# Kernel optimization log

Hardware: AMD Instinct MI355X
Metric: run time of the kernel (lower is better)

The kernel has to match this reference:

```python
import jax, jax.numpy as jnp
from jax import lax
import numpy as np

B, N, H, T, NPB = 1024, 50, 128, 50, 3
C_TANH, NEG = 10.0, 1e9


def _lstm(x, h, c, Wi, Wh, b):
    gates = x @ Wi + h @ Wh + b
    i, f, g, o = jnp.split(gates, 4, axis=-1)
    c2 = jax.nn.sigmoid(f) * c + jax.nn.sigmoid(i) * jnp.tanh(g)
    return jax.nn.sigmoid(o) * jnp.tanh(c2), c2


def setup_inputs() -> dict:
    key = jax.random.key(0)
    ks = jax.random.split(key, 20)
    rn = lambda k, shape, fan: (jax.random.normal(k, shape, jnp.float32) / np.float32(np.sqrt(fan)))
    return {
        'input_pnt': jax.random.uniform(ks[0], (B, N, 2), jnp.float32),
        'W_emb': rn(ks[1], (2, H), 2), 'b_emb': jnp.zeros((H,), jnp.float32),
        'dec_init': rn(ks[2], (1, 1, H), H),
        'Wi': rn(ks[3], (H, 4 * H), H), 'Wh': rn(ks[4], (H, 4 * H), H), 'b_lstm': jnp.zeros((4 * H,), jnp.float32),
        'Wq_g': rn(ks[5], (H, H), H), 'Wref_g': rn(ks[6], (H, H), H), 'v_g': rn(ks[7], (H,), H),
        'Wq_p': rn(ks[8], (H, H), H), 'Wref_p': rn(ks[9], (H, H), H), 'v_p': rn(ks[10], (H,), H),
        'Wi_c': rn(ks[11], (H, 4 * H), H), 'Wh_c': rn(ks[12], (H, 4 * H), H), 'b_c': jnp.zeros((4 * H,), jnp.float32),
        'Wq_c': rn(ks[13], (H, H), H), 'Wref_c': rn(ks[14], (H, H), H), 'v_c': rn(ks[15], (H,), H),
        'W1': rn(ks[16], (H, H), H), 'b1': jnp.zeros((H,), jnp.float32),
        'W2': rn(ks[17], (H, 1), H), 'b2': jnp.zeros((1,), jnp.float32),
    }


def _forward(input_pnt, W_emb, b_emb, dec_init, Wi, Wh, b_lstm, Wq_g, Wref_g, v_g,
             Wq_p, Wref_p, v_p, Wi_c, Wh_c, b_c, Wq_c, Wref_c, v_c, W1, b1, W2, b2):
    context = input_pnt @ W_emb + b_emb                    # [B,N,H] embedded nodes
    e_g = context @ Wref_g                                  # glimpse keys (step-invariant, hoisted)
    e_p = context @ Wref_p                                  # pointer keys (hoisted)
    z = jnp.zeros((B, H), context.dtype)
    carry0 = (z, z, jnp.zeros((B, N), context.dtype), jnp.broadcast_to(dec_init[0, 0], (B, H)))

    def step(carry, _):
        h, c, mask, dec_in = carry
        h2, c2 = _lstm(dec_in, h, c, Wi, Wh, b_lstm)
        # glimpse attention (masked)
        q = h2 @ Wq_g
        u = jnp.einsum('bnh,h->bn', jnp.tanh(e_g + q[:, None, :]), v_g) - NEG * mask
        g = jnp.einsum('bn,bnh->bh', jax.nn.softmax(u, -1), e_g)
        # pointer attention with tanh exploration clipping (masked)
        u2 = jnp.einsum('bnh,h->bn', jnp.tanh(e_p + (g @ Wq_p)[:, None, :]), v_p)
        logit = C_TANH * jnp.tanh(u2) - NEG * mask
        logprob = jax.nn.log_softmax(logit, -1)
        prob = jax.nn.softmax(logit, -1)
        action = jnp.argmax(prob, -1)                       # greedy decode
        mask2 = jnp.maximum(mask, jax.nn.one_hot(action, N, dtype=mask.dtype))
        dec_next = jnp.take_along_axis(context, action[:, None, None], axis=1)[:, 0]
        coords = jnp.take_along_axis(input_pnt, action[:, None, None], axis=1)[:, 0]
        return (h2, c2, mask2, dec_next), (logprob, prob, action, coords)

    (_, _, _, dec_last), (logprobs, probs, actions, coords) = lax.scan(step, carry0, None, length=T)
    logprobs = jnp.transpose(logprobs, (1, 0, 2))           # [B,T,N]
    probs = jnp.transpose(probs, (1, 0, 2))
    actions = jnp.transpose(actions, (1, 0))                # [B,T]
    coords = jnp.transpose(coords, (1, 0, 2))               # [B,T,2] visited coordinates
    # reward: TSP tour length
    seg = coords[:, 1:] - coords[:, :-1]
    close = coords[:, 0] - coords[:, -1]
    R = jnp.sum(jnp.sqrt(jnp.sum(seg * seg, -1) + 1e-10), -1) + jnp.sqrt(jnp.sum(close * close, -1) + 1e-10)
    # critic: one LSTM step on last action broadcast to hidden, cn[0], then process blocks
    a4c = jnp.broadcast_to(actions[:, -1].astype(context.dtype)[:, None], (B, H))
    _, hy = _lstm(a4c, z, z, Wi_c, Wh_c, b_c)
    enc = dec_last[:, None, :]                              # context gathered at last action, [B,1,H]
    e_c = enc @ Wref_c
    for _ in range(NPB):
        u = jnp.einsum('bnh,h->bn', jnp.tanh(e_c + (hy @ Wq_c)[:, None, :]), v_c)
        hy = jnp.einsum('bn,bnh->bh', jax.nn.softmax(C_TANH * jnp.tanh(u), -1), e_c)
    v = (jax.nn.relu(hy @ W1 + b1) @ W2 + b2)[:, 0]
    return R, v, logprobs, actions, coords, probs


def reference(input_pnt, W_emb, b_emb, dec_init, Wi, Wh, b_lstm, Wq_g, Wref_g, v_g,
              Wq_p, Wref_p, v_p, Wi_c, Wh_c, b_c, Wq_c, Wref_c, v_c, W1, b1, W2, b2):
    return _forward(input_pnt, W_emb, b_emb, dec_init, Wi, Wh, b_lstm, Wq_g, Wref_g, v_g,
                    Wq_p, Wref_p, v_p, Wi_c, Wh_c, b_c, Wq_c, Wref_c, v_c, W1, b1, W2, b2)
```

## Files before the change

kernel.cpp:

```cpp
#include <hip/hip_runtime.h>
#include <math.h>

#define Bsz 1024
#define Npt 50
#define Hd 128
#define G4 512
#define Tt 50
#define NEGC 1000000000.0f
#define CTANH 10.0f

#define OFF_R 0
#define OFF_V 1024
#define OFF_LP 2048
#define OFF_A 2562048
#define OFF_C 2613248
#define OFF_P 2715648

#define WS_TG 0
#define WS_TP 512
#define WS_TQ 1024
#define WS_A0 1536
#define WS_A1 2048
#define WS_A2 2560
#define WS_A3 3072
#define WS_CT 3584

__device__ __forceinline__ float fsig(float x) {
  return __builtin_amdgcn_rcpf(1.0f + __expf(-x));
}

__device__ __forceinline__ float ftanh(float x) {
  float e = __expf(2.0f * x);
  return 1.0f - 2.0f * __builtin_amdgcn_rcpf(e + 1.0f);
}

__device__ __forceinline__ float dpp_sum_bcast(float x) {
  int v;
  v = __builtin_amdgcn_update_dpp(0, __float_as_int(x), 0x111, 0xf, 0xf, true);
  x += __int_as_float(v);
  v = __builtin_amdgcn_update_dpp(0, __float_as_int(x), 0x112, 0xf, 0xf, true);
  x += __int_as_float(v);
  v = __builtin_amdgcn_update_dpp(0, __float_as_int(x), 0x114, 0xf, 0xf, true);
  x += __int_as_float(v);
  v = __builtin_amdgcn_update_dpp(0, __float_as_int(x), 0x118, 0xf, 0xf, true);
  x += __int_as_float(v);
  v = __builtin_amdgcn_update_dpp(0, __float_as_int(x), 0x142, 0xf, 0xf, true);
  x += __int_as_float(v);
  v = __builtin_amdgcn_update_dpp(0, __float_as_int(x), 0x143, 0xf, 0xf, true);
  x += __int_as_float(v);
  return __int_as_float(__builtin_amdgcn_readlane(__float_as_int(x), 63));
}

__device__ __forceinline__ float dpp_max_bcast(float x) {
  int v;
  v = __builtin_amdgcn_update_dpp(0, __float_as_int(x), 0x111, 0xf, 0xf, true);
  x = fmaxf(x, __int_as_float(v));
  v = __builtin_amdgcn_update_dpp(0, __float_as_int(x), 0x112, 0xf, 0xf, true);
  x = fmaxf(x, __int_as_float(v));
  v = __builtin_amdgcn_update_dpp(0, __float_as_int(x), 0x114, 0xf, 0xf, true);
  x = fmaxf(x, __int_as_float(v));
  v = __builtin_amdgcn_update_dpp(0, __float_as_int(x), 0x118, 0xf, 0xf, true);
  x = fmaxf(x, __int_as_float(v));
  v = __builtin_amdgcn_update_dpp(0, __float_as_int(x), 0x142, 0xf, 0xf, true);
  x = fmaxf(x, __int_as_float(v));
  v = __builtin_amdgcn_update_dpp(0, __float_as_int(x), 0x143, 0xf, 0xf, true);
  x = fmaxf(x, __int_as_float(v));
  return __int_as_float(__builtin_amdgcn_readlane(__float_as_int(x), 63));
}

__device__ __forceinline__ float xsum(float x) {
  #pragma unroll
  for (int off = 32; off >= 1; off >>= 1) x += __shfl_xor(x, off, 64);
  return x;
}

__global__ __launch_bounds__(512) void k_pre(const float* __restrict__ Wemb,
                                             const float* __restrict__ bemb,
                                             const float* __restrict__ dinit,
                                             const float* __restrict__ Wi,
                                             const float* __restrict__ bl,
                                             const float* __restrict__ Wqp,
                                             const float* __restrict__ Wrg,
                                             const float* __restrict__ Wrp,
                                             const float* __restrict__ vg,
                                             const float* __restrict__ vp,
                                             const float* __restrict__ Wrc,
                                             const float* __restrict__ W1,
                                             const float* __restrict__ b1,
                                             const float* __restrict__ W2,
                                             float* __restrict__ ws) {
  __shared__ float mg_s[2][128], mp_s[2][128], cg_s[128], cp_s[128];
  __shared__ float pg_s[2][128], pc_s[128];
  __shared__ float r0_s[128], r1_s[128], rc_s[128];
  int t = threadIdx.x;
  if (t < 256) {
    int j = t >> 7, hh = t & 127;
    float ag = 0.f, ap = 0.f;
    for (int k = 0; k < 128; ++k) {
      float we = Wemb[j * 128 + k];
      ag = fmaf(we, Wrg[k * 128 + hh], ag);
      ap = fmaf(we, Wrp[k * 128 + hh], ap);
    }
    mg_s[j][hh] = ag; mp_s[j][hh] = ap;
  } else if (t < 384) {
    int hh = t & 127;
    float cgv = 0.f, cpv = 0.f;
    for (int k = 0; k < 128; ++k) {
      float be = bemb[k];
      cgv = fmaf(be, Wrg[k * 128 + hh], cgv);
      cpv = fmaf(be, Wrp[k * 128 + hh], cpv);
    }
    cg_s[hh] = cgv; cp_s[hh] = cpv;
  } else {
    int hh = t & 127;
    float a0 = 0.f, a1 = 0.f, ac = 0.f;
    for (int k = 0; k < 128; ++k) {
      float wr = Wrc[k * 128 + hh];
      a0 = fmaf(Wemb[k], wr, a0);
      a1 = fmaf(Wemb[128 + k], wr, a1);
      ac = fmaf(bemb[k], wr, ac);
    }
    r0_s[hh] = a0; r1_s[hh] = a1; rc_s[hh] = ac;
  }
  __syncthreads();
  if (t < 256) {
    int j = t >> 7, hh = t & 127;
    float pg = 0.f;
    for (int k = 0; k < 128; ++k) pg = fmaf(mg_s[j][k], Wqp[k * 128 + hh], pg);
    pg_s[j][hh] = pg;
  } else if (t < 384) {
    int hh = t & 127;
    float pcv = 0.f;
    for (int k = 0; k < 128; ++k) pcv = fmaf(cg_s[k], Wqp[k * 128 + hh], pcv);
    pc_s[hh] = pcv + cp_s[hh];
  } else {
    int hh = t & 127;
    float t0 = 0.f, t1 = 0.f, tc = 0.f;
    for (int k = 0; k < 128; ++k) {
      float w1 = W1[k * 128 + hh];
      t0 = fmaf(r0_s[k], w1, t0);
      t1 = fmaf(r1_s[k], w1, t1);
      tc = fmaf(rc_s[k], w1, tc);
    }
    float4* w4 = (float4*)ws;
    w4[WS_CT / 4 + hh] = make_float4(t0, t1, tc + b1[hh], W2[hh]);
  }
  __syncthreads();
  if (t < 128) {
    float4* w4 = (float4*)ws;
    w4[WS_TG / 4 + t] = make_float4(mg_s[0][t], mg_s[1][t], vg[t], cg_s[t]);
    w4[WS_TP / 4 + t] = make_float4(mp_s[0][t], mp_s[1][t], vp[t], cp_s[t]);
    w4[WS_TQ / 4 + t] = make_float4(pg_s[0][t], pg_s[1][t], pc_s[t], 0.f);
  }
  {
    int j = t;
    float a0 = 0.f, a1 = 0.f, a2 = 0.f, a3 = 0.f;
    for (int k = 0; k < 128; ++k) {
      float wi = Wi[k * G4 + j];
      a0 = fmaf(Wemb[k], wi, a0);
      a1 = fmaf(Wemb[128 + k], wi, a1);
      a2 = fmaf(bemb[k], wi, a2);
      a3 = fmaf(dinit[k], wi, a3);
    }
    ws[WS_A0 + j] = a0;
    ws[WS_A1 + j] = a1;
    ws[WS_A2 + j] = a2 + bl[j];
    ws[WS_A3 + j] = a3 + bl[j];
  }
}

__global__ __launch_bounds__(1024, 4) void k_mega(const float* __restrict__ ip,
                                                  const float* __restrict__ Wh,
                                                  const float* __restrict__ Wqg,
                                                  const float* __restrict__ b2,
                                                  const float* __restrict__ ws,
                                                  float* __restrict__ out) {
  __shared__ __align__(16) float gpart[8][4][G4];
  __shared__ __align__(16) float qpart[8][4][Hd];
  __shared__ __align__(16) float up_s[4][4][64];
  __shared__ __align__(16) float up2_s[4][4][64];
  __shared__ __align__(16) float qc_s[4][Hd];
  __shared__ __align__(16) float h_s[4][Hd];
  __shared__ __align__(16) float c_s[4][Hd];
  __shared__ __align__(16) float tg_s[G4];
  __shared__ __align__(16) float tp_s[G4];
  __shared__ __align__(16) float tq_s[G4];
  __shared__ __align__(16) float ct_s[G4];
  __shared__ __align__(16) float a0_s[G4], a1_s[G4], a2_s[G4], a3_s[G4];
  __shared__ float vsum_s[2][4];
  __shared__ __align__(16) float ip_s[4][Npt * 2];
  __shared__ float mask_s[4][Npt];
  __shared__ float ch_s[4][Npt * 2];
  __shared__ float sel_s[4][2];

  int t = threadIdx.x, blk = blockIdx.x;
  int w = t >> 6, lane = t & 63;
  int kh = t >> 7, jt = t & 127;

  float4 wv[16];
  #pragma unroll
  for (int j = 0; j < 16; ++j)
    wv[j] = *(const float4*)&Wh[(kh * 16 + j) * G4 + jt * 4];
  float wqr[16];
  #pragma unroll
  for (int j = 0; j < 16; ++j)
    wqr[j] = Wqg[(kh * 16 + j) * Hd + jt];

  const float4* ws4 = (const float4*)ws;
  if (t < 128) {
    float4 g4 = ws4[WS_TG / 4 + t];
    ((float4*)tg_s)[t] = make_float4(2.f * g4.x, 2.f * g4.y, -2.f * g4.z, 2.f * g4.w);
    float4 p4 = ws4[WS_TP / 4 + t];
    ((float4*)tp_s)[t] = make_float4(2.f * p4.x, 2.f * p4.y, -2.f * p4.z, 0.f);
    float4 q4 = ws4[WS_TQ / 4 + t];
    ((float4*)tq_s)[t] = make_float4(2.f * q4.x, 2.f * q4.y, 2.f * q4.z, 0.f);
    ((float4*)ct_s)[t] = ws4[WS_CT / 4 + t];
  } else if (t < 256) {
    int i = t - 128;
    ((float4*)a0_s)[i] = ((const float4*)(ws + WS_A0))[i];
    ((float4*)a1_s)[i] = ((const float4*)(ws + WS_A1))[i];
    ((float4*)a2_s)[i] = ((const float4*)(ws + WS_A2))[i];
    ((float4*)a3_s)[i] = ((const float4*)(ws + WS_A3))[i];
  }
  if (t < 200) {
    ((float2*)ip_s)[t] = ((const float2*)ip)[blk * 200 + t];
    ((float*)mask_s)[t] = 0.f;
  }
  if (t < 512) {
    int r = t >> 7, hh = t & 127;
    h_s[r][hh] = 0.f;
    c_s[r][hh] = 0.f;
  }
  if (t < 8) {
    int which = t >> 2, c = t & 3;
    float s = 0.f;
    for (int hp = 0; hp < 32; ++hp)
      s += ws[(which ? WS_TP : WS_TG) + (c * 32 + hp) * 4 + 2];
    vsum_s[which][c] = s;
  }
  if (t < 8) ((float*)sel_s)[t] = 0.f;
  __syncthreads();

  int cr = w & 3, hc = w >> 2;
  float2 pn = make_float2(0.f, 0.f);
  if (lane < Npt) pn = ((float2*)ip_s)[cr * Npt + lane];

  for (int s = 0; s < Tt; ++s) {
    {
      int k0 = kh * 16;
      #pragma unroll
      for (int r = 0; r < 4; ++r) {
        float hv[16];
        #pragma unroll
        for (int q4i = 0; q4i < 4; ++q4i)
          *(float4*)&hv[q4i * 4] = *(const float4*)&h_s[r][k0 + q4i * 4];
        float a0 = 0.f, a1 = 0.f, a2 = 0.f, a3 = 0.f;
        #pragma unroll
        for (int kk = 0; kk < 16; ++kk) {
          float4 wj = wv[kk];
          a0 = fmaf(hv[kk], wj.x, a0);
          a1 = fmaf(hv[kk], wj.y, a1);
          a2 = fmaf(hv[kk], wj.z, a2);
          a3 = fmaf(hv[kk], wj.w, a3);
        }
        *(float4*)&gpart[kh][r][jt * 4] = make_float4(a0, a1, a2, a3);
      }
      if (w >= 12 && s > 0) {
        int row = cr, stp = s - 1, b = blk * 4 + row;
        float u = up2_s[0][row][lane] + up2_s[1][row][lane]
                + up2_s[2][row][lane] + up2_s[3][row][lane];
        float x = 0.f, e = 0.f;
        if (lane < Npt) {
          x = CTANH * ftanh(u) - NEGC * mask_s[row][lane];
          e = __expf(x);
        }
        float ssum = dpp_sum_bcast(e);
        float ls = __logf(ssum);
        float prob = e * __builtin_amdgcn_rcpf(ssum);
        if (lane < Npt) {
          out[OFF_LP + ((size_t)b * Tt + stp) * Npt + lane] = x - ls;
          out[OFF_P + ((size_t)b * Tt + stp) * Npt + lane] = prob;
        }
        float mx = dpp_max_bcast(prob);
        unsigned long long bal = __ballot((prob == mx) && (lane < Npt));
        int a = __ffsll(bal) - 1;
        float p0a = ip_s[row][2 * a];
        float p1a = ip_s[row][2 * a + 1];
        if (lane == 0) {
          out[OFF_A + (size_t)b * Tt + stp] = (float)a;
          out[OFF_C + ((size_t)b * Tt + stp) * 2 + 0] = p0a;
          out[OFF_C + ((size_t)b * Tt + stp) * 2 + 1] = p1a;
          ((float2*)ch_s)[row * Npt + stp] = make_float2(p0a, p1a);
          mask_s[row][a] = 1.0f;
          sel_s[row][0] = p0a;
          sel_s[row][1] = p1a;
        }
      }
    }
    __syncthreads();
    if (t < 512) {
      int r = t >> 7, hh = t & 127;
      float p0 = sel_s[r][0], p1 = sel_s[r][1];
      float g[4];
      #pragma unroll
      for (int gi = 0; gi < 4; ++gi) {
        int j = gi * 128 + hh;
        float x = (s == 0) ? a3_s[j]
                           : fmaf(p0, a0_s[j], fmaf(p1, a1_s[j], a2_s[j]));
        #pragma unroll
        for (int k8 = 0; k8 < 8; ++k8) x += gpart[k8][r][j];
        g[gi] = x;
      }
      float c2 = fsig(g[1]) * c_s[r][hh] + fsig(g[0]) * ftanh(g[2]);
      float h2 = fsig(g[3]) * ftanh(c2);
      c_s[r][hh] = c2;
      h_s[r][hh] = h2;
    }
    __syncthreads();
    {
      int k0 = kh * 16;
      #pragma unroll
      for (int r = 0; r < 4; ++r) {
        float hv[16];
        #pragma unroll
        for (int q4i = 0; q4i < 4; ++q4i)
          *(float4*)&hv[q4i * 4] = *(const float4*)&h_s[r][k0 + q4i * 4];
        float a = 0.f;
        #pragma unroll
        for (int kk = 0; kk < 16; ++kk) a = fmaf(hv[kk], wqr[kk], a);
        qpart[kh][r][jt] = a;
      }
    }
    __syncthreads();
    {
      if (lane < 32) {
        int h = hc * 32 + lane;
        float qs = ((float4*)tg_s)[h].w
                 + 2.f * (qpart[0][cr][h] + qpart[1][cr][h] + qpart[2][cr][h]
                        + qpart[3][cr][h] + qpart[4][cr][h] + qpart[5][cr][h]
                        + qpart[6][cr][h] + qpart[7][cr][h]);
        qc_s[cr][h] = qs;
      }
      float ac = vsum_s[0][hc];
      #pragma unroll 8
      for (int hp = 0; hp < 32; ++hp) {
        int h = hc * 32 + hp;
        float4 tg4 = ((float4*)tg_s)[h];
        float a = fmaf(pn.x, tg4.x, fmaf(pn.y, tg4.y, qc_s[cr][h]));
        ac = fmaf(tg4.z, __builtin_amdgcn_rcpf(__expf(a) + 1.0f), ac);
      }
      up_s[hc][cr][lane] = ac;
    }
    __syncthreads();
    {
      float u = up_s[0][cr][lane] + up_s[1][cr][lane]
              + up_s[2][cr][lane] + up_s[3][cr][lane];
      float e = 0.f;
      if (lane < Npt) e = __expf(u - NEGC * mask_s[cr][lane]);
      float ssum = dpp_sum_bcast(e);
      float sx = dpp_sum_bcast(e * pn.x);
      float sy = dpp_sum_bcast(e * pn.y);
      float inv = __builtin_amdgcn_rcpf(ssum);
      float s0 = sx * inv;
      float s1 = sy * inv;
      if (lane < 32) {
        int h = hc * 32 + lane;
        float4 tq4 = ((float4*)tq_s)[h];
        qc_s[cr][h] = fmaf(s0, tq4.x, fmaf(s1, tq4.y, tq4.z));
      }
      float ac = vsum_s[1][hc];
      #pragma unroll 8
      for (int hp = 0; hp < 32; ++hp) {
        int h = hc * 32 + hp;
        float4 tp4 = ((float4*)tp_s)[h];
        float a = fmaf(pn.x, tp4.x, fmaf(pn.y, tp4.y, qc_s[cr][h]));
        ac = fmaf(tp4.z, __builtin_amdgcn_rcpf(__expf(a) + 1.0f), ac);
      }
      up2_s[hc][cr][lane] = ac;
    }
    __syncthreads();
  }

  if (w >= 12) {
    int row = cr, stp = Tt - 1, b = blk * 4 + row;
    float u = up2_s[0][row][lane] + up2_s[1][row][lane]
            + up2_s[2][row][lane] + up2_s[3][row][lane];
    float x = 0.f, e = 0.f;
    if (lane < Npt) {
      x = CTANH * ftanh(u) - NEGC * mask_s[row][lane];
      e = __expf(x);
    }
    float ssum = dpp_sum_bcast(e);
    float ls = __logf(ssum);
    float prob = e * __builtin_amdgcn_rcpf(ssum);
    if (lane < Npt) {
      out[OFF_LP + ((size_t)b * Tt + stp) * Npt + lane] = x - ls;
      out[OFF_P + ((size_t)b * Tt + stp) * Npt + lane] = prob;
    }
    float mx = dpp_max_bcast(prob);
    unsigned long long bal = __ballot((prob == mx) && (lane < Npt));
    int a = __ffsll(bal) - 1;
    float p0a = ip_s[row][2 * a];
    float p1a = ip_s[row][2 * a + 1];
    if (lane == 0) {
      out[OFF_A + (size_t)b * Tt + stp] = (float)a;
      out[OFF_C + ((size_t)b * Tt + stp) * 2 + 0] = p0a;
      out[OFF_C + ((size_t)b * Tt + stp) * 2 + 1] = p1a;
      ((float2*)ch_s)[row * Npt + stp] = make_float2(p0a, p1a);
      sel_s[row][0] = p0a;
      sel_s[row][1] = p1a;
    }
  }
  __syncthreads();

  if (w < 4) {
    int r = w, b = blk * 4 + r;
    float p0 = sel_s[r][0], p1 = sel_s[r][1];
    float4 ct0 = ((float4*)ct_s)[lane];
    float4 ct1 = ((float4*)ct_s)[64 + lane];
    float t1a = fmaxf(fmaf(p0, ct0.x, fmaf(p1, ct0.y, ct0.z)), 0.f);
    float t1b = fmaxf(fmaf(p0, ct1.x, fmaf(p1, ct1.y, ct1.z)), 0.f);
    float sv = xsum(t1a * ct0.w + t1b * ct1.w);
    if (lane == 0) out[OFF_V + b] = sv + b2[0];
    float rr = 0.f;
    if (lane < Npt) {
      float2 c0 = ((float2*)ch_s)[r * Npt + lane];
      float2 c1 = ((float2*)ch_s)[r * Npt + ((lane == Npt - 1) ? 0 : lane + 1)];
      float dx = c1.x - c0.x, dy = c1.y - c0.y;
      rr = sqrtf(dx * dx + dy * dy + 1e-10f);
    }
    rr = xsum(rr);
    if (lane == 0) out[OFF_R + b] = rr;
  }
}

extern "C" void kernel_launch(void* const* d_in, const int* in_sizes, int n_in,
                              void* d_out, int out_size, void* d_ws, size_t ws_size,
                              hipStream_t stream) {
  (void)in_sizes; (void)n_in; (void)out_size; (void)ws_size;
  const float* ip    = (const float*)d_in[0];
  const float* Wemb  = (const float*)d_in[1];
  const float* bemb  = (const float*)d_in[2];
  const float* dinit = (const float*)d_in[3];
  const float* Wi    = (const float*)d_in[4];
  const float* Wh    = (const float*)d_in[5];
  const float* bl    = (const float*)d_in[6];
  const float* Wqg   = (const float*)d_in[7];
  const float* Wrg   = (const float*)d_in[8];
  const float* vg    = (const float*)d_in[9];
  const float* Wqp   = (const float*)d_in[10];
  const float* Wrp   = (const float*)d_in[11];
  const float* vp    = (const float*)d_in[12];
  const float* Wrc   = (const float*)d_in[17];
  const float* W1    = (const float*)d_in[19];
  const float* b1    = (const float*)d_in[20];
  const float* W2    = (const float*)d_in[21];
  const float* b2    = (const float*)d_in[22];
  float* out = (float*)d_out;
  float* ws  = (float*)d_ws;

  k_pre<<<1, 512, 0, stream>>>(Wemb, bemb, dinit, Wi, bl, Wqp, Wrg, Wrp,
                               vg, vp, Wrc, W1, b1, W2, ws);
  k_mega<<<256, 1024, 0, stream>>>(ip, Wh, Wqg, b2, ws, out);
}
```

Measured before the change: 626.0 us.

## Split 4-row block into two interleaved 2-row groups to overlap decode phases

The per-step decode loop is restructured so the four batch rows per block form two groups of two. Each group's LSTM, query, glimpse, pointer and selection phases are staggered against the other's, so the phases run concurrently across barriers instead of serially. The aim is to shorten the serial critical path per step, since each phase previously left most waves idle. The number of barriers per step stays at four, but each phase now handles half the rows with twice the attention partition width. The scheduling becomes more intricate, and ordering errors between groups are a correctness risk.

```diff
diff --git a/kernel.cpp b/kernel.cpp
--- a/kernel.cpp
+++ b/kernel.cpp
@@ -175,10 +175,10 @@
                                                   const float* __restrict__ b2,
                                                   const float* __restrict__ ws,
                                                   float* __restrict__ out) {
-  __shared__ __align__(16) float gpart[8][4][G4];
-  __shared__ __align__(16) float qpart[8][4][Hd];
-  __shared__ __align__(16) float up_s[4][4][64];
-  __shared__ __align__(16) float up2_s[4][4][64];
+  __shared__ __align__(16) float gpart[8][2][G4];
+  __shared__ __align__(16) float qpart[8][2][Hd];
+  __shared__ __align__(16) float up_s[8][2][64];
+  __shared__ __align__(16) float up2_s[8][2][64];
   __shared__ __align__(16) float qc_s[4][Hd];
   __shared__ __align__(16) float h_s[4][Hd];
   __shared__ __align__(16) float c_s[4][Hd];
@@ -187,7 +187,7 @@
   __shared__ __align__(16) float tq_s[G4];
   __shared__ __align__(16) float ct_s[G4];
   __shared__ __align__(16) float a0_s[G4], a1_s[G4], a2_s[G4], a3_s[G4];
-  __shared__ float vsum_s[2][4];
+  __shared__ float vsum_s[2][8];
   __shared__ __align__(16) float ip_s[4][Npt * 2];
   __shared__ float mask_s[4][Npt];
   __shared__ float ch_s[4][Npt * 2];
@@ -231,186 +231,193 @@
     h_s[r][hh] = 0.f;
     c_s[r][hh] = 0.f;
   }
-  if (t < 8) {
-    int which = t >> 2, c = t & 3;
-    float s = 0.f;
-    for (int hp = 0; hp < 32; ++hp)
-      s += ws[(which ? WS_TP : WS_TG) + (c * 32 + hp) * 4 + 2];
-    vsum_s[which][c] = s;
+  if (t < 16) {
+    int which = t >> 3, c = t & 7;
+    float sv = 0.f;
+    for (int hp = 0; hp < 16; ++hp)
+      sv += ws[(which ? WS_TP : WS_TG) + (c * 16 + hp) * 4 + 2];
+    vsum_s[which][c] = sv;
   }
   if (t < 8) ((float*)sel_s)[t] = 0.f;
   __syncthreads();
 
-  int cr = w & 3, hc = w >> 2;
-  float2 pn = make_float2(0.f, 0.f);
-  if (lane < Npt) pn = ((float2*)ip_s)[cr * Npt + lane];
-
-  for (int s = 0; s < Tt; ++s) {
-    {
-      int k0 = kh * 16;
+  float2 pnA = make_float2(0.f, 0.f), pnB = make_float2(0.f, 0.f);
+  if (lane < Npt) {
+    pnA = ((float2*)ip_s)[(w & 1) * Npt + lane];
+    pnB = ((float2*)ip_s)[(2 + (w & 1)) * Npt + lane];
+  }
+
+  auto A1f = [&](int base) {
+    int k0 = kh * 16;
+    #pragma unroll
+    for (int r = 0; r < 2; ++r) {
+      float hv[16];
       #pragma unroll
-      for (int r = 0; r < 4; ++r) {
-        float hv[16];
-        #pragma unroll
-        for (int q4i = 0; q4i < 4; ++q4i)
-          *(float4*)&hv[q4i * 4] = *(const float4*)&h_s[r][k0 + q4i * 4];
-        float a0 = 0.f, a1 = 0.f, a2 = 0.f, a3 = 0.f;
-        #pragma unroll
-        for (int kk = 0; kk < 16; ++kk) {
-          float4 wj = wv[kk];
-          a0 = fmaf(hv[kk], wj.x, a0);
-          a1 = fmaf(hv[kk], wj.y, a1);
-          a2 = fmaf(hv[kk], wj.z, a2);
-          a3 = fmaf(hv[kk], wj.w, a3);
-        }
-        *(float4*)&gpart[kh][r][jt * 4] = make_float4(a0, a1, a2, a3);
+      for (int q4i = 0; q4i < 4; ++q4i)
+        *(float4*)&hv[q4i * 4] = *(const float4*)&h_s[base + r][k0 + q4i * 4];
+      float a0 = 0.f, a1 = 0.f, a2 = 0.f, a3 = 0.f;
+      #pragma unroll
+      for (int kk = 0; kk < 16; ++kk) {
+        float4 wj = wv[kk];
+        a0 = fmaf(hv[kk], wj.x, a0);
+        a1 = fmaf(hv[kk], wj.y, a1);
+        a2 = fmaf(hv[kk], wj.z, a2);
+        a3 = fmaf(hv[kk], wj.w, a3);
       }
-      if (w >= 12 && s > 0) {
-        int row = cr, stp = s - 1, b = blk * 4 + row;
-        float u = up2_s[0][row][lane] + up2_s[1][row][lane]
-                + up2_s[2][row][lane] + up2_s[3][row][lane];
-        float x = 0.f, e = 0.f;
-        if (lane < Npt) {
-          x = CTANH * ftanh(u) - NEGC * mask_s[row][lane];
-          e = __expf(x);
-        }
-        float ssum = dpp_sum_bcast(e);
-        float ls = __logf(ssum);
-        float prob = e * __builtin_amdgcn_rcpf(ssum);
-        if (lane < Npt) {
-          out[OFF_LP + ((size_t)b * Tt + stp) * Npt + lane] = x - ls;
-          out[OFF_P + ((size_t)b * Tt + stp) * Npt + lane] = prob;
-        }
-        float mx = dpp_max_bcast(prob);
-        unsigned long long bal = __ballot((prob == mx) && (lane < Npt));
-        int a = __ffsll(bal) - 1;
-        float p0a = ip_s[row][2 * a];
-        float p1a = ip_s[row][2 * a + 1];
-        if (lane == 0) {
-          out[OFF_A + (size_t)b * Tt + stp] = (float)a;
-          out[OFF_C + ((size_t)b * Tt + stp) * 2 + 0] = p0a;
-          out[OFF_C + ((size_t)b * Tt + stp) * 2 + 1] = p1a;
-          ((float2*)ch_s)[row * Npt + stp] = make_float2(p0a, p1a);
-          mask_s[row][a] = 1.0f;
-          sel_s[row][0] = p0a;
-          sel_s[row][1] = p1a;
-        }
-      }
-    }
-    __syncthreads();
-    if (t < 512) {
-      int r = t >> 7, hh = t & 127;
-      float p0 = sel_s[r][0], p1 = sel_s[r][1];
+      *(float4*)&gpart[kh][r][jt * 4] = make_float4(a0, a1, a2, a3);
+    }
+  };
+
+  auto P2f = [&](int base, int stp) {
+    if (t < 256) {
+      int r = t >> 7, hh = t & 127, gr = base + r;
+      float p0 = sel_s[gr][0], p1 = sel_s[gr][1];
       float g[4];
       #pragma unroll
       for (int gi = 0; gi < 4; ++gi) {
         int j = gi * 128 + hh;
-        float x = (s == 0) ? a3_s[j]
-                           : fmaf(p0, a0_s[j], fmaf(p1, a1_s[j], a2_s[j]));
+        float x = (stp == 0) ? a3_s[j]
+                             : fmaf(p0, a0_s[j], fmaf(p1, a1_s[j], a2_s[j]));
         #pragma unroll
         for (int k8 = 0; k8 < 8; ++k8) x += gpart[k8][r][j];
         g[gi] = x;
       }
-      float c2 = fsig(g[1]) * c_s[r][hh] + fsig(g[0]) * ftanh(g[2]);
+      float c2 = fsig(g[1]) * c_s[gr][hh] + fsig(g[0]) * ftanh(g[2]);
       float h2 = fsig(g[3]) * ftanh(c2);
-      c_s[r][hh] = c2;
-      h_s[r][hh] = h2;
-    }
+      c_s[gr][hh] = c2;
+      h_s[gr][hh] = h2;
+    }
+  };
+
+  auto P3f = [&](int base) {
+    int k0 = kh * 16;
+    #pragma unroll
+    for (int r = 0; r < 2; ++r) {
+      float hv[16];
+      #pragma unroll
+      for (int q4i = 0; q4i < 4; ++q4i)
+        *(float4*)&hv[q4i * 4] = *(const float4*)&h_s[base + r][k0 + q4i * 4];
+      float a = 0.f;
+      #pragma unroll
+      for (int kk = 0; kk < 16; ++kk) a = fmaf(hv[kk], wqr[kk], a);
+      qpart[kh][r][jt] = a;
+    }
+  };
+
+  auto P4f = [&](int base) {
+    int cr = w & 1, hc = w >> 1, gr = base + cr;
+    float2 pn = base ? pnB : pnA;
+    if (lane < 16) {
+      int h = hc * 16 + lane;
+      float qs = ((float4*)tg_s)[h].w
+               + 2.f * (qpart[0][cr][h] + qpart[1][cr][h] + qpart[2][cr][h]
+                      + qpart[3][cr][h] + qpart[4][cr][h] + qpart[5][cr][h]
+                      + qpart[6][cr][h] + qpart[7][cr][h]);
+      qc_s[gr][h] = qs;
+    }
+    float ac = vsum_s[0][hc];
+    #pragma unroll
+    for (int hp = 0; hp < 16; ++hp) {
+      int h = hc * 16 + hp;
+      float4 tg4 = ((float4*)tg_s)[h];
+      float a = fmaf(pn.x, tg4.x, fmaf(pn.y, tg4.y, qc_s[gr][h]));
+      ac = fmaf(tg4.z, __builtin_amdgcn_rcpf(__expf(a) + 1.0f), ac);
+    }
+    up_s[hc][cr][lane] = ac;
+  };
+
+  auto P5f = [&](int base) {
+    int cr = w & 1, hc = w >> 1, gr = base + cr;
+    float2 pn = base ? pnB : pnA;
+    float u = up_s[0][cr][lane] + up_s[1][cr][lane]
+            + up_s[2][cr][lane] + up_s[3][cr][lane]
+            + up_s[4][cr][lane] + up_s[5][cr][lane]
+            + up_s[6][cr][lane] + up_s[7][cr][lane];
+    float e = 0.f;
+    if (lane < Npt) e = __expf(u - NEGC * mask_s[gr][lane]);
+    float ssum = dpp_sum_bcast(e);
+    float sx = dpp_sum_bcast(e * pn.x);
+    float sy = dpp_sum_bcast(e * pn.y);
+    float inv = __builtin_amdgcn_rcpf(ssum);
+    float s0 = sx * inv;
+    float s1 = sy * inv;
+    if (lane < 16) {
+      int h = hc * 16 + lane;
+      float4 tq4 = ((float4*)tq_s)[h];
+      qc_s[gr][h] = fmaf(s0, tq4.x, fmaf(s1, tq4.y, tq4.z));
+    }
+    float ac = vsum_s[1][hc];
+    #pragma unroll
+    for (int hp = 0; hp < 16; ++hp) {
+      int h = hc * 16 + hp;
+      float4 tp4 = ((float4*)tp_s)[h];
+      float a = fmaf(pn.x, tp4.x, fmaf(pn.y, tp4.y, qc_s[gr][h]));
+      ac = fmaf(tp4.z, __builtin_amdgcn_rcpf(__expf(a) + 1.0f), ac);
+    }
+    up2_s[hc][cr][lane] = ac;
+  };
+
+  auto Ff = [&](int base, int stp) {
+    if (w >= 14) {
+      int row = w & 1, gr = base + row, b = blk * 4 + gr;
+      float u = up2_s[0][row][lane] + up2_s[1][row][lane]
+              + up2_s[2][row][lane] + up2_s[3][row][lane]
+              + up2_s[4][row][lane] + up2_s[5][row][lane]
+              + up2_s[6][row][lane] + up2_s[7][row][lane];
+      float x = 0.f, e = 0.f;
+      if (lane < Npt) {
+        x = CTANH * ftanh(u) - NEGC * mask_s[gr][lane];
+        e = __expf(x);
+      }
+      float ssum = dpp_sum_bcast(e);
+      float ls = __logf(ssum);
+      float prob = e * __builtin_amdgcn_rcpf(ssum);
+      if (lane < Npt) {
+        out[OFF_LP + ((size_t)b * Tt + stp) * Npt + lane] = x - ls;
+        out[OFF_P + ((size_t)b * Tt + stp) * Npt + lane] = prob;
+      }
+      float mx = dpp_max_bcast(prob);
+      unsigned long long bal = __ballot((prob == mx) && (lane < Npt));
+      int a = __ffsll(bal) - 1;
+      float p0a = ip_s[gr][2 * a];
+      float p1a = ip_s[gr][2 * a + 1];
+      if (lane == 0) {
+        out[OFF_A + (size_t)b * Tt + stp] = (float)a;
+        out[OFF_C + ((size_t)b * Tt + stp) * 2 + 0] = p0a;
+        out[OFF_C + ((size_t)b * Tt + stp) * 2 + 1] = p1a;
+        ((float2*)ch_s)[gr * Npt + stp] = make_float2(p0a, p1a);
+        mask_s[gr][a] = 1.0f;
+        sel_s[gr][0] = p0a;
+        sel_s[gr][1] = p1a;
+      }
+    }
+  };
+
+  for (int s = 0; s < Tt; ++s) {
+    A1f(0);
+    if (s > 0) { P4f(2); Ff(0, s - 1); }
     __syncthreads();
-    {
-      int k0 = kh * 16;
-      #pragma unroll
-      for (int r = 0; r < 4; ++r) {
-        float hv[16];
-        #pragma unroll
-        for (int q4i = 0; q4i < 4; ++q4i)
-          *(float4*)&hv[q4i * 4] = *(const float4*)&h_s[r][k0 + q4i * 4];
-        float a = 0.f;
-        #pragma unroll
-        for (int kk = 0; kk < 16; ++kk) a = fmaf(hv[kk], wqr[kk], a);
-        qpart[kh][r][jt] = a;
-      }
-    }
+    P2f(0, s);
+    if (s > 0) P5f(2);
     __syncthreads();
-    {
-      if (lane < 32) {
-        int h = hc * 32 + lane;
-        float qs = ((float4*)tg_s)[h].w
-                 + 2.f * (qpart[0][cr][h] + qpart[1][cr][h] + qpart[2][cr][h]
-                        + qpart[3][cr][h] + qpart[4][cr][h] + qpart[5][cr][h]
-                        + qpart[6][cr][h] + qpart[7][cr][h]);
-        qc_s[cr][h] = qs;
-      }
-      float ac = vsum_s[0][hc];
-      #pragma unroll 8
-      for (int hp = 0; hp < 32; ++hp) {
-        int h = hc * 32 + hp;
-        float4 tg4 = ((float4*)tg_s)[h];
-        float a = fmaf(pn.x, tg4.x, fmaf(pn.y, tg4.y, qc_s[cr][h]));
-        ac = fmaf(tg4.z, __builtin_amdgcn_rcpf(__expf(a) + 1.0f), ac);
-      }
-      up_s[hc][cr][lane] = ac;
-    }
+    P3f(0);
+    A1f(2);
+    if (s > 0) Ff(2, s - 1);
     __syncthreads();
-    {
-      float u = up_s[0][cr][lane] + up_s[1][cr][lane]
-              + up_s[2][cr][lane] + up_s[3][cr][lane];
-      float e = 0.f;
-      if (lane < Npt) e = __expf(u - NEGC * mask_s[cr][lane]);
-      float ssum = dpp_sum_bcast(e);
-      float sx = dpp_sum_bcast(e * pn.x);
-      float sy = dpp_sum_bcast(e * pn.y);
-      float inv = __builtin_amdgcn_rcpf(ssum);
-      float s0 = sx * inv;
-      float s1 = sy * inv;
-      if (lane < 32) {
-        int h = hc * 32 + lane;
-        float4 tq4 = ((float4*)tq_s)[h];
-        qc_s[cr][h] = fmaf(s0, tq4.x, fmaf(s1, tq4.y, tq4.z));
-      }
-      float ac = vsum_s[1][hc];
-      #pragma unroll 8
-      for (int hp = 0; hp < 32; ++hp) {
-        int h = hc * 32 + hp;
-        float4 tp4 = ((float4*)tp_s)[h];
-        float a = fmaf(pn.x, tp4.x, fmaf(pn.y, tp4.y, qc_s[cr][h]));
-        ac = fmaf(tp4.z, __builtin_amdgcn_rcpf(__expf(a) + 1.0f), ac);
-      }
-      up2_s[hc][cr][lane] = ac;
-    }
+    P4f(0);
+    P2f(2, s);
     __syncthreads();
-  }
-
-  if (w >= 12) {
-    int row = cr, stp = Tt - 1, b = blk * 4 + row;
-    float u = up2_s[0][row][lane] + up2_s[1][row][lane]
-            + up2_s[2][row][lane] + up2_s[3][row][lane];
-    float x = 0.f, e = 0.f;
-    if (lane < Npt) {
-      x = CTANH * ftanh(u) - NEGC * mask_s[row][lane];
-      e = __expf(x);
-    }
-    float ssum = dpp_sum_bcast(e);
-    float ls = __logf(ssum);
-    float prob = e * __builtin_amdgcn_rcpf(ssum);
-    if (lane < Npt) {
-      out[OFF_LP + ((size_t)b * Tt + stp) * Npt + lane] = x - ls;
-      out[OFF_P + ((size_t)b * Tt + stp) * Npt + lane] = prob;
-    }
-    float mx = dpp_max_bcast(prob);
-    unsigned long long bal = __ballot((prob == mx) && (lane < Npt));
-    int a = __ffsll(bal) - 1;
-    float p0a = ip_s[row][2 * a];
-    float p1a = ip_s[row][2 * a + 1];
-    if (lane == 0) {
-      out[OFF_A + (size_t)b * Tt + stp] = (float)a;
-      out[OFF_C + ((size_t)b * Tt + stp) * 2 + 0] = p0a;
-      out[OFF_C + ((size_t)b * Tt + stp) * 2 + 1] = p1a;
-      ((float2*)ch_s)[row * Npt + stp] = make_float2(p0a, p1a);
-      sel_s[row][0] = p0a;
-      sel_s[row][1] = p1a;
-    }
-  }
+    P5f(0);
+    P3f(2);
+    __syncthreads();
+  }
+
+  P4f(2);
+  Ff(0, Tt - 1);
+  __syncthreads();
+  P5f(2);
+  __syncthreads();
+  Ff(2, Tt - 1);
   __syncthreads();
 
   if (w < 4) {
```

Result: slower. 771.7 us (+23.3%).

## Halve rows per block, 512-thread blocks, stream Wh from global memory

Applied to the files above, without the earlier changes.

Each block now handles 2 batch rows with 512 threads instead of 4 rows with 1024 threads, and the launch doubles to 512 blocks. The Wh recurrent weights are no longer held in registers. Each step re-reads them from global or L2 memory, and each warp covers 16 k-rows across all 512 gate columns for both rows. The aim is to free registers and shared memory so more blocks fit per CU and wavefronts sit less at barriers. The cost is heavy repeated weight traffic on every time step.

```diff
diff --git a/kernel.cpp b/kernel.cpp
--- a/kernel.cpp
+++ b/kernel.cpp
@@ -169,42 +169,38 @@
   }
 }
 
-__global__ __launch_bounds__(1024, 4) void k_mega(const float* __restrict__ ip,
-                                                  const float* __restrict__ Wh,
-                                                  const float* __restrict__ Wqg,
-                                                  const float* __restrict__ b2,
-                                                  const float* __restrict__ ws,
-                                                  float* __restrict__ out) {
-  __shared__ __align__(16) float gpart[8][4][G4];
-  __shared__ __align__(16) float qpart[8][4][Hd];
-  __shared__ __align__(16) float up_s[4][4][64];
-  __shared__ __align__(16) float up2_s[4][4][64];
-  __shared__ __align__(16) float qc_s[4][Hd];
-  __shared__ __align__(16) float h_s[4][Hd];
-  __shared__ __align__(16) float c_s[4][Hd];
+__global__ __launch_bounds__(512, 4) void k_mega(const float* __restrict__ ip,
+                                                 const float* __restrict__ Wh,
+                                                 const float* __restrict__ Wqg,
+                                                 const float* __restrict__ b2,
+                                                 const float* __restrict__ ws,
+                                                 float* __restrict__ out) {
+  __shared__ __align__(16) float gpart[8][2][G4];
+  __shared__ __align__(16) float qpart[8][2][Hd];
+  __shared__ __align__(16) float up_s[4][2][64];
+  __shared__ __align__(16) float up2_s[4][2][64];
+  __shared__ __align__(16) float qc_s[2][Hd];
+  __shared__ __align__(16) float h_s[2][Hd];
+  __shared__ __align__(16) float c_s[2][Hd];
   __shared__ __align__(16) float tg_s[G4];
   __shared__ __align__(16) float tp_s[G4];
   __shared__ __align__(16) float tq_s[G4];
   __shared__ __align__(16) float ct_s[G4];
   __shared__ __align__(16) float a0_s[G4], a1_s[G4], a2_s[G4], a3_s[G4];
   __shared__ float vsum_s[2][4];
-  __shared__ __align__(16) float ip_s[4][Npt * 2];
-  __shared__ float mask_s[4][Npt];
-  __shared__ float ch_s[4][Npt * 2];
-  __shared__ float sel_s[4][2];
+  __shared__ __align__(16) float ip_s[2][Npt * 2];
+  __shared__ float mask_s[2][Npt];
+  __shared__ float ch_s[2][Npt * 2];
+  __shared__ float sel_s[2][2];
 
   int t = threadIdx.x, blk = blockIdx.x;
   int w = t >> 6, lane = t & 63;
-  int kh = t >> 7, jt = t & 127;
-
-  float4 wv[16];
+  int k0 = w * 16;
+
+  float wqr[32];
   #pragma unroll
-  for (int j = 0; j < 16; ++j)
-    wv[j] = *(const float4*)&Wh[(kh * 16 + j) * G4 + jt * 4];
-  float wqr[16];
-  #pragma unroll
-  for (int j = 0; j < 16; ++j)
-    wqr[j] = Wqg[(kh * 16 + j) * Hd + jt];
+  for (int kk = 0; kk < 16; ++kk)
+    *(float2*)&wqr[2 * kk] = *(const float2*)&Wqg[(k0 + kk) * Hd + lane * 2];
 
   const float4* ws4 = (const float4*)ws;
   if (t < 128) {
@@ -222,51 +218,64 @@
     ((float4*)a2_s)[i] = ((const float4*)(ws + WS_A2))[i];
     ((float4*)a3_s)[i] = ((const float4*)(ws + WS_A3))[i];
   }
-  if (t < 200) {
-    ((float2*)ip_s)[t] = ((const float2*)ip)[blk * 200 + t];
+  if (t < 100) {
+    ((float2*)ip_s)[t] = ((const float2*)ip)[blk * 100 + t];
     ((float*)mask_s)[t] = 0.f;
   }
-  if (t < 512) {
+  if (t < 256) {
     int r = t >> 7, hh = t & 127;
     h_s[r][hh] = 0.f;
     c_s[r][hh] = 0.f;
   }
   if (t < 8) {
     int which = t >> 2, c = t & 3;
-    float s = 0.f;
+    float sv = 0.f;
     for (int hp = 0; hp < 32; ++hp)
-      s += ws[(which ? WS_TP : WS_TG) + (c * 32 + hp) * 4 + 2];
-    vsum_s[which][c] = s;
-  }
-  if (t < 8) ((float*)sel_s)[t] = 0.f;
+      sv += ws[(which ? WS_TP : WS_TG) + (c * 32 + hp) * 4 + 2];
+    vsum_s[which][c] = sv;
+  }
+  if (t < 4) ((float*)sel_s)[t] = 0.f;
   __syncthreads();
 
-  int cr = w & 3, hc = w >> 2;
+  int cr = w & 1, hc = w >> 1;
   float2 pn = make_float2(0.f, 0.f);
   if (lane < Npt) pn = ((float2*)ip_s)[cr * Npt + lane];
+  int cA = lane * 4, cB = 256 + lane * 4;
+  const float4* Wh4 = (const float4*)Wh;
 
   for (int s = 0; s < Tt; ++s) {
     {
-      int k0 = kh * 16;
+      float hv0[16], hv1[16];
       #pragma unroll
-      for (int r = 0; r < 4; ++r) {
-        float hv[16];
-        #pragma unroll
-        for (int q4i = 0; q4i < 4; ++q4i)
-          *(float4*)&hv[q4i * 4] = *(const float4*)&h_s[r][k0 + q4i * 4];
-        float a0 = 0.f, a1 = 0.f, a2 = 0.f, a3 = 0.f;
-        #pragma unroll
-        for (int kk = 0; kk < 16; ++kk) {
-          float4 wj = wv[kk];
-          a0 = fmaf(hv[kk], wj.x, a0);
-          a1 = fmaf(hv[kk], wj.y, a1);
-          a2 = fmaf(hv[kk], wj.z, a2);
-          a3 = fmaf(hv[kk], wj.w, a3);
-        }
-        *(float4*)&gpart[kh][r][jt * 4] = make_float4(a0, a1, a2, a3);
-      }
-      if (w >= 12 && s > 0) {
-        int row = cr, stp = s - 1, b = blk * 4 + row;
+      for (int q4i = 0; q4i < 4; ++q4i) {
+        *(float4*)&hv0[q4i * 4] = *(const float4*)&h_s[0][k0 + q4i * 4];
+        *(float4*)&hv1[q4i * 4] = *(const float4*)&h_s[1][k0 + q4i * 4];
+      }
+      float4 a00 = make_float4(0.f, 0.f, 0.f, 0.f);
+      float4 a01 = make_float4(0.f, 0.f, 0.f, 0.f);
+      float4 a10 = make_float4(0.f, 0.f, 0.f, 0.f);
+      float4 a11 = make_float4(0.f, 0.f, 0.f, 0.f);
+      #pragma unroll
+      for (int kk = 0; kk < 16; ++kk) {
+        float4 wA = Wh4[((k0 + kk) * G4 + cA) >> 2];
+        float4 wB = Wh4[((k0 + kk) * G4 + cB) >> 2];
+        float h0 = hv0[kk], h1 = hv1[kk];
+        a00.x = fmaf(h0, wA.x, a00.x); a00.y = fmaf(h0, wA.y, a00.y);
+        a00.z = fmaf(h0, wA.z, a00.z); a00.w = fmaf(h0, wA.w, a00.w);
+        a01.x = fmaf(h0, wB.x, a01.x); a01.y = fmaf(h0, wB.y, a01.y);
+        a01.z = fmaf(h0, wB.z, a01.z); a01.w = fmaf(h0, wB.w, a01.w);
+        a10.x = fmaf(h1, wA.x, a10.x); a10.y = fmaf(h1, wA.y, a10.y);
+        a10.z = fmaf(h1, wA.z, a10.z); a10.w = fmaf(h1, wA.w, a10.w);
+        a11.x = fmaf(h1, wB.x, a11.x); a11.y = fmaf(h1, wB.y, a11.y);
+        a11.z = fmaf(h1, wB.z, a11.z); a11.w = fmaf(h1, wB.w, a11.w);
+      }
+      *(float4*)&gpart[w][0][cA] = a00;
+      *(float4*)&gpart[w][0][cB] = a01;
+      *(float4*)&gpart[w][1][cA] = a10;
+      *(float4*)&gpart[w][1][cB] = a11;
+
+      if (w >= 6 && s > 0) {
+        int row = w & 1, stp = s - 1, b = blk * 2 + row;
         float u = up2_s[0][row][lane] + up2_s[1][row][lane]
                 + up2_s[2][row][lane] + up2_s[3][row][lane];
         float x = 0.f, e = 0.f;
@@ -298,7 +307,7 @@
       }
     }
     __syncthreads();
-    if (t < 512) {
+    if (t < 256) {
       int r = t >> 7, hh = t & 127;
       float p0 = sel_s[r][0], p1 = sel_s[r][1];
       float g[4];
@@ -318,18 +327,22 @@
     }
     __syncthreads();
     {
-      int k0 = kh * 16;
+      float hv0[16], hv1[16];
       #pragma unroll
-      for (int r = 0; r < 4; ++r) {
-        float hv[16];
-        #pragma unroll
-        for (int q4i = 0; q4i < 4; ++q4i)
-          *(float4*)&hv[q4i * 4] = *(const float4*)&h_s[r][k0 + q4i * 4];
-        float a = 0.f;
-        #pragma unroll
-        for (int kk = 0; kk < 16; ++kk) a = fmaf(hv[kk], wqr[kk], a);
-        qpart[kh][r][jt] = a;
-      }
+      for (int q4i = 0; q4i < 4; ++q4i) {
+        *(float4*)&hv0[q4i * 4] = *(const float4*)&h_s[0][k0 + q4i * 4];
+        *(float4*)&hv1[q4i * 4] = *(const float4*)&h_s[1][k0 + q4i * 4];
+      }
+      float q00 = 0.f, q01 = 0.f, q10 = 0.f, q11 = 0.f;
+      #pragma unroll
+      for (int kk = 0; kk < 16; ++kk) {
+        q00 = fmaf(hv0[kk], wqr[2 * kk], q00);
+        q01 = fmaf(hv0[kk], wqr[2 * kk + 1], q01);
+        q10 = fmaf(hv1[kk], wqr[2 * kk], q10);
+        q11 = fmaf(hv1[kk], wqr[2 * kk + 1], q11);
+      }
+      *(float2*)&qpart[w][0][lane * 2] = make_float2(q00, q01);
+      *(float2*)&qpart[w][1][lane * 2] = make_float2(q10, q11);
     }
     __syncthreads();
     {
@@ -381,8 +394,8 @@
     __syncthreads();
   }
 
-  if (w >= 12) {
-    int row = cr, stp = Tt - 1, b = blk * 4 + row;
+  if (w >= 6) {
+    int row = w & 1, stp = Tt - 1, b = blk * 2 + row;
     float u = up2_s[0][row][lane] + up2_s[1][row][lane]
             + up2_s[2][row][lane] + up2_s[3][row][lane];
     float x = 0.f, e = 0.f;
@@ -413,8 +426,8 @@
   }
   __syncthreads();
 
-  if (w < 4) {
-    int r = w, b = blk * 4 + r;
+  if (w < 2) {
+    int r = w, b = blk * 2 + r;
     float p0 = sel_s[r][0], p1 = sel_s[r][1];
     float4 ct0 = ((float4*)ct_s)[lane];
     float4 ct1 = ((float4*)ct_s)[64 + lane];
@@ -461,5 +474,5 @@
 
   k_pre<<<1, 512, 0, stream>>>(Wemb, bemb, dinit, Wi, bl, Wqp, Wrg, Wrp,
                                vg, vp, Wrc, W1, b1, W2, ws);
-  k_mega<<<256, 1024, 0, stream>>>(ip, Wh, Wqg, b2, ws, out);
-}
+  k_mega<<<512, 512, 0, stream>>>(ip, Wh, Wqg, b2, ws, out);
+}
```

New measurement: 2.393 ms. 3.82x slower.

## Replace block barriers with per-row LDS counters and skew LSTM matvec across attention

Applied to the files above, without the earlier changes.

Two of the block-wide __syncthreads in each decode step become per-row barriers built from LDS atomic counters. Only the four waves that handle the same batch row now wait for each other. The Wh gate matvec for the next step is split by row and interleaved around the attention phases so waves can fill idle time. The pointer softmax/argmax now runs inside the same step rather than being deferred to the start of the next one. This adds spin-wait polling with s_sleep and relies on the ordering of the partial gpart writes being correct across rows. gpart is zero-initialised, apparently to cover the rows whose matvec is not issued on the final step.

```diff
diff --git a/kernel.cpp b/kernel.cpp
--- a/kernel.cpp
+++ b/kernel.cpp
@@ -192,10 +192,12 @@
   __shared__ float mask_s[4][Npt];
   __shared__ float ch_s[4][Npt * 2];
   __shared__ float sel_s[4][2];
+  __shared__ int ctr_s[4];
 
   int t = threadIdx.x, blk = blockIdx.x;
   int w = t >> 6, lane = t & 63;
   int kh = t >> 7, jt = t & 127;
+  int k0q = kh * 16;
 
   float4 wv[16];
   #pragma unroll
@@ -233,70 +235,53 @@
   }
   if (t < 8) {
     int which = t >> 2, c = t & 3;
-    float s = 0.f;
+    float sv = 0.f;
     for (int hp = 0; hp < 32; ++hp)
-      s += ws[(which ? WS_TP : WS_TG) + (c * 32 + hp) * 4 + 2];
-    vsum_s[which][c] = s;
+      sv += ws[(which ? WS_TP : WS_TG) + (c * 32 + hp) * 4 + 2];
+    vsum_s[which][c] = sv;
   }
   if (t < 8) ((float*)sel_s)[t] = 0.f;
+  if (t < 4) ctr_s[t] = 0;
+  {
+    float4 z4 = make_float4(0.f, 0.f, 0.f, 0.f);
+    #pragma unroll
+    for (int i = 0; i < 4; ++i) ((float4*)gpart)[t * 4 + i] = z4;
+  }
   __syncthreads();
 
   int cr = w & 3, hc = w >> 2;
   float2 pn = make_float2(0.f, 0.f);
   if (lane < Npt) pn = ((float2*)ip_s)[cr * Npt + lane];
 
+  int lt = 0;
+  auto lsync = [&]() {
+    lt += 4;
+    if (lane == 0)
+      __hip_atomic_fetch_add(&ctr_s[cr], 1, __ATOMIC_RELEASE,
+                             __HIP_MEMORY_SCOPE_WORKGROUP);
+    while (__hip_atomic_load(&ctr_s[cr], __ATOMIC_ACQUIRE,
+                             __HIP_MEMORY_SCOPE_WORKGROUP) < lt)
+      __builtin_amdgcn_s_sleep(1);
+  };
+
+  auto A1row = [&](int r) {
+    float hv[16];
+    #pragma unroll
+    for (int q4i = 0; q4i < 4; ++q4i)
+      *(float4*)&hv[q4i * 4] = *(const float4*)&h_s[r][k0q + q4i * 4];
+    float a0 = 0.f, a1 = 0.f, a2 = 0.f, a3 = 0.f;
+    #pragma unroll
+    for (int kk = 0; kk < 16; ++kk) {
+      float4 wj = wv[kk];
+      a0 = fmaf(hv[kk], wj.x, a0);
+      a1 = fmaf(hv[kk], wj.y, a1);
+      a2 = fmaf(hv[kk], wj.z, a2);
+      a3 = fmaf(hv[kk], wj.w, a3);
+    }
+    *(float4*)&gpart[kh][r][jt * 4] = make_float4(a0, a1, a2, a3);
+  };
+
   for (int s = 0; s < Tt; ++s) {
-    {
-      int k0 = kh * 16;
-      #pragma unroll
-      for (int r = 0; r < 4; ++r) {
-        float hv[16];
-        #pragma unroll
-        for (int q4i = 0; q4i < 4; ++q4i)
-          *(float4*)&hv[q4i * 4] = *(const float4*)&h_s[r][k0 + q4i * 4];
-        float a0 = 0.f, a1 = 0.f, a2 = 0.f, a3 = 0.f;
-        #pragma unroll
-        for (int kk = 0; kk < 16; ++kk) {
-          float4 wj = wv[kk];
-          a0 = fmaf(hv[kk], wj.x, a0);
-          a1 = fmaf(hv[kk], wj.y, a1);
-          a2 = fmaf(hv[kk], wj.z, a2);
-          a3 = fmaf(hv[kk], wj.w, a3);
-        }
-        *(float4*)&gpart[kh][r][jt * 4] = make_float4(a0, a1, a2, a3);
-      }
-      if (w >= 12 && s > 0) {
-        int row = cr, stp = s - 1, b = blk * 4 + row;
-        float u = up2_s[0][row][lane] + up2_s[1][row][lane]
-                + up2_s[2][row][lane] + up2_s[3][row][lane];
-        float x = 0.f, e = 0.f;
-        if (lane < Npt) {
-          x = CTANH * ftanh(u) - NEGC * mask_s[row][lane];
-          e = __expf(x);
-        }
-        float ssum = dpp_sum_bcast(e);
-        float ls = __logf(ssum);
-        float prob = e * __builtin_amdgcn_rcpf(ssum);
-        if (lane < Npt) {
-          out[OFF_LP + ((size_t)b * Tt + stp) * Npt + lane] = x - ls;
-          out[OFF_P + ((size_t)b * Tt + stp) * Npt + lane] = prob;
-        }
-        float mx = dpp_max_bcast(prob);
-        unsigned long long bal = __ballot((prob == mx) && (lane < Npt));
-        int a = __ffsll(bal) - 1;
-        float p0a = ip_s[row][2 * a];
-        float p1a = ip_s[row][2 * a + 1];
-        if (lane == 0) {
-          out[OFF_A + (size_t)b * Tt + stp] = (float)a;
-          out[OFF_C + ((size_t)b * Tt + stp) * 2 + 0] = p0a;
-          out[OFF_C + ((size_t)b * Tt + stp) * 2 + 1] = p1a;
-          ((float2*)ch_s)[row * Npt + stp] = make_float2(p0a, p1a);
-          mask_s[row][a] = 1.0f;
-          sel_s[row][0] = p0a;
-          sel_s[row][1] = p1a;
-        }
-      }
-    }
     __syncthreads();
     if (t < 512) {
       int r = t >> 7, hh = t & 127;
@@ -318,13 +303,12 @@
     }
     __syncthreads();
     {
-      int k0 = kh * 16;
       #pragma unroll
       for (int r = 0; r < 4; ++r) {
         float hv[16];
         #pragma unroll
         for (int q4i = 0; q4i < 4; ++q4i)
-          *(float4*)&hv[q4i * 4] = *(const float4*)&h_s[r][k0 + q4i * 4];
+          *(float4*)&hv[q4i * 4] = *(const float4*)&h_s[r][k0q + q4i * 4];
         float a = 0.f;
         #pragma unroll
         for (int kk = 0; kk < 16; ++kk) a = fmaf(hv[kk], wqr[kk], a);
@@ -332,6 +316,9 @@
       }
     }
     __syncthreads();
+    if (s + 1 < Tt) {
+      for (int r = 0; r < cr; ++r) A1row(r);
+    }
     {
       if (lane < 32) {
         int h = hc * 32 + lane;
@@ -351,7 +338,7 @@
       }
       up_s[hc][cr][lane] = ac;
     }
-    __syncthreads();
+    lsync();
     {
       float u = up_s[0][cr][lane] + up_s[1][cr][lane]
               + up_s[2][cr][lane] + up_s[3][cr][lane];
@@ -378,37 +365,40 @@
       }
       up2_s[hc][cr][lane] = ac;
     }
-    __syncthreads();
-  }
-
-  if (w >= 12) {
-    int row = cr, stp = Tt - 1, b = blk * 4 + row;
-    float u = up2_s[0][row][lane] + up2_s[1][row][lane]
-            + up2_s[2][row][lane] + up2_s[3][row][lane];
-    float x = 0.f, e = 0.f;
-    if (lane < Npt) {
-      x = CTANH * ftanh(u) - NEGC * mask_s[row][lane];
-      e = __expf(x);
-    }
-    float ssum = dpp_sum_bcast(e);
-    float ls = __logf(ssum);
-    float prob = e * __builtin_amdgcn_rcpf(ssum);
-    if (lane < Npt) {
-      out[OFF_LP + ((size_t)b * Tt + stp) * Npt + lane] = x - ls;
-      out[OFF_P + ((size_t)b * Tt + stp) * Npt + lane] = prob;
-    }
-    float mx = dpp_max_bcast(prob);
-    unsigned long long bal = __ballot((prob == mx) && (lane < Npt));
-    int a = __ffsll(bal) - 1;
-    float p0a = ip_s[row][2 * a];
-    float p1a = ip_s[row][2 * a + 1];
-    if (lane == 0) {
-      out[OFF_A + (size_t)b * Tt + stp] = (float)a;
-      out[OFF_C + ((size_t)b * Tt + stp) * 2 + 0] = p0a;
-      out[OFF_C + ((size_t)b * Tt + stp) * 2 + 1] = p1a;
-      ((float2*)ch_s)[row * Npt + stp] = make_float2(p0a, p1a);
-      sel_s[row][0] = p0a;
-      sel_s[row][1] = p1a;
+    lsync();
+    if (hc == 3) {
+      int row = cr, b = blk * 4 + row;
+      float u = up2_s[0][row][lane] + up2_s[1][row][lane]
+              + up2_s[2][row][lane] + up2_s[3][row][lane];
+      float x = 0.f, e = 0.f;
+      if (lane < Npt) {
+        x = CTANH * ftanh(u) - NEGC * mask_s[row][lane];
+        e = __expf(x);
+      }
+      float ssum = dpp_sum_bcast(e);
+      float ls = __logf(ssum);
+      float prob = e * __builtin_amdgcn_rcpf(ssum);
+      if (lane < Npt) {
+        out[OFF_LP + ((size_t)b * Tt + s) * Npt + lane] = x - ls;
+        out[OFF_P + ((size_t)b * Tt + s) * Npt + lane] = prob;
+      }
+      float mx = dpp_max_bcast(prob);
+      unsigned long long bal = __ballot((prob == mx) && (lane < Npt));
+      int a = __ffsll(bal) - 1;
+      float p0a = ip_s[row][2 * a];
+      float p1a = ip_s[row][2 * a + 1];
+      if (lane == 0) {
+        out[OFF_A + (size_t)b * Tt + s] = (float)a;
+        out[OFF_C + ((size_t)b * Tt + s) * 2 + 0] = p0a;
+        out[OFF_C + ((size_t)b * Tt + s) * 2 + 1] = p1a;
+        ((float2*)ch_s)[row * Npt + s] = make_float2(p0a, p1a);
+        mask_s[row][a] = 1.0f;
+        sel_s[row][0] = p0a;
+        sel_s[row][1] = p1a;
+      }
+    }
+    if (s + 1 < Tt) {
+      for (int r = cr; r < 4; ++r) A1row(r);
     }
   }
   __syncthreads();
```

Result: slower. 653.3 us (+4.4%).
